# Kernel optimization log

Measured on AMD Instinct MI355X. Metric: run time of the kernel, lower is better.

The kernel has to match this reference:

```python
import jax, jax.numpy as jnp
import numpy as np

T, B = 256, 64
VOCAB, EMBED, HIDDEN, LAYERS, TAGS = 50000, 512, 512, 2, 9
H = HIDDEN // 2  # per-direction hidden size


def setup_inputs() -> dict:
    key = jax.random.key(0)
    ks = jax.random.split(key, 11)
    s = 0.05
    embed_table = jax.random.normal(ks[1], (VOCAB, EMBED), dtype=jnp.float32) * s
    embed_table = embed_table.at[0].set(0.0)  # padding_idx=0 row is zero
    return {
        "x": jax.random.randint(ks[0], (T, B), 1, VOCAB),  # ids >=1 -> full lengths
        "embed_table": embed_table,
        "w_ih": jax.random.normal(ks[2], (LAYERS, 2, 4 * H, HIDDEN), dtype=jnp.float32) * s,
        "w_hh": jax.random.normal(ks[3], (LAYERS, 2, 4 * H, H), dtype=jnp.float32) * s,
        "b_ih": jax.random.normal(ks[4], (LAYERS, 2, 4 * H), dtype=jnp.float32) * s,
        "b_hh": jax.random.normal(ks[5], (LAYERS, 2, 4 * H), dtype=jnp.float32) * s,
        "out_w": jax.random.normal(ks[6], (TAGS, HIDDEN), dtype=jnp.float32) * s,
        "out_b": jax.random.normal(ks[7], (TAGS,), dtype=jnp.float32) * s,
        "start_trans": jax.random.normal(ks[8], (TAGS,), dtype=jnp.float32) * s,
        "end_trans": jax.random.normal(ks[9], (TAGS,), dtype=jnp.float32) * s,
        "trans": jax.random.normal(ks[10], (TAGS, TAGS), dtype=jnp.float32) * s,
    }


def _lstm_dir(xs, Wih, Whh, b, reverse):
    """One LSTM direction over time-major xs [T,B,D]; PyTorch gate order i,f,g,o."""
    bsz = xs.shape[1]
    h0 = jnp.zeros((bsz, H), xs.dtype)
    c0 = jnp.zeros((bsz, H), xs.dtype)

    def step(carry, xt):
        h, c = carry
        g = xt @ Wih.T + h @ Whh.T + b
        i, f, gg, o = jnp.split(g, 4, axis=-1)
        c = jax.nn.sigmoid(f) * c + jax.nn.sigmoid(i) * jnp.tanh(gg)
        h = jax.nn.sigmoid(o) * jnp.tanh(c)
        return (h, c), h

    _, hs = jax.lax.scan(step, (h0, c0), xs, reverse=reverse)
    return hs  # [T,B,H], aligned to input time order


def _emissions(x, embed_table, w_ih, w_hh, b_ih, b_hh, out_w, out_b):
    seq = embed_table[x]  # [T,B,EMBED]
    for l in range(LAYERS):
        fwd = _lstm_dir(seq, w_ih[l, 0], w_hh[l, 0], b_ih[l, 0] + b_hh[l, 0], False)
        bwd = _lstm_dir(seq, w_ih[l, 1], w_hh[l, 1], b_ih[l, 1] + b_hh[l, 1], True)
        seq = jnp.concatenate([fwd, bwd], axis=-1)  # [T,B,HIDDEN]
    return seq @ out_w.T + out_b  # [T,B,TAGS]


def reference(x, embed_table, w_ih, w_hh, b_ih, b_hh, out_w, out_b,
              start_trans, end_trans, trans):
    em = _emissions(x, embed_table, w_ih, w_hh, b_ih, b_hh, out_w, out_b)

    # Viterbi decode (all sequences full-length since ids >= 1)
    score0 = start_trans[None, :] + em[0]  # [B,TAGS]

    def vstep(score, em_t):
        tot = score[:, :, None] + trans[None, :, :]  # [B,prev,cur]
        best_prev = jnp.argmax(tot, axis=1)          # [B,cur]
        return jnp.max(tot, axis=1) + em_t, best_prev

    score, history = jax.lax.scan(vstep, score0, em[1:])  # history: [T-1,B,TAGS]
    score = score + end_trans[None, :]
    best_last = jnp.argmax(score, axis=-1)   # [B]
    best_score = jnp.max(score, axis=-1)     # [B]

    def btstep(tag, idx_t):
        prev = jnp.take_along_axis(idx_t, tag[:, None], axis=1)[:, 0]
        return prev, prev

    _, prevs = jax.lax.scan(btstep, best_last, history, reverse=True)  # [T-1,B]
    tags = jnp.concatenate([prevs, best_last[None, :]], axis=0)        # [T,B]
    return tags.T, best_score  # ([B,T] best paths, [B] path scores)
```

## Files before the change

### kernel.cpp

```cpp
#include <hip/hip_runtime.h>
#include <math.h>

#define TAGS 9

static __device__ __forceinline__ float sigmoidf_(float x) {
  return 1.0f / (1.0f + expf(-x));
}

__device__ __forceinline__ float4 ld4_sc(const float* p) {
  float4 r;
  asm volatile("global_load_dwordx4 %0, %1, off sc0 sc1" : "=v"(r) : "v"(p) : "memory");
  return r;
}
__device__ __forceinline__ void st1_sc(float* p, float v) {
  asm volatile("global_store_dword %0, %1, off sc0 sc1" :: "v"(p), "v"(v) : "memory");
}
__device__ __forceinline__ void waitcnt0() {
  asm volatile("s_waitcnt vmcnt(0)" ::: "memory");
}

__global__ void k_gather(const int* __restrict__ x, const float* __restrict__ table,
                         float* __restrict__ seq) {
  int tid = blockIdx.x * 256 + threadIdx.x;
  int row = tid >> 7;
  int e4 = tid & 127;
  int idx = x[row];
  const float4* src = (const float4*)(table + (size_t)idx * 512);
  float4* dst = (float4*)(seq + (size_t)row * 512);
  dst[e4] = src[e4];
}

__global__ __launch_bounds__(256, 2)
void k_gemm_gates(const float* __restrict__ A, const float* __restrict__ B,
                  const float* __restrict__ bias1, const float* __restrict__ bias2,
                  float* __restrict__ gatesT) {
  __shared__ float As[16][132];
  __shared__ float Bs[16][132];
  int tid = threadIdx.x;
  int tx = tid & 15, ty = tid >> 4;
  int n0 = blockIdx.x * 128, m0 = blockIdx.y * 128;
  int lr = tid >> 2;
  int lk = (tid & 3) * 4;
  float acc[8][8];
#pragma unroll
  for (int i = 0; i < 8; i++)
#pragma unroll
    for (int j = 0; j < 8; j++) acc[i][j] = 0.f;
  const float* Ab = A + (size_t)m0 * 512;
  const float* Bb = B + (size_t)n0 * 512;
  for (int k0 = 0; k0 < 512; k0 += 16) {
    float4 a0 = *(const float4*)&Ab[(size_t)lr * 512 + k0 + lk];
    float4 a1 = *(const float4*)&Ab[(size_t)(lr + 64) * 512 + k0 + lk];
    float4 w0 = *(const float4*)&Bb[(size_t)lr * 512 + k0 + lk];
    float4 w1 = *(const float4*)&Bb[(size_t)(lr + 64) * 512 + k0 + lk];
    __syncthreads();
    As[lk + 0][lr] = a0.x; As[lk + 1][lr] = a0.y; As[lk + 2][lr] = a0.z; As[lk + 3][lr] = a0.w;
    As[lk + 0][lr + 64] = a1.x; As[lk + 1][lr + 64] = a1.y; As[lk + 2][lr + 64] = a1.z; As[lk + 3][lr + 64] = a1.w;
    Bs[lk + 0][lr] = w0.x; Bs[lk + 1][lr] = w0.y; Bs[lk + 2][lr] = w0.z; Bs[lk + 3][lr] = w0.w;
    Bs[lk + 0][lr + 64] = w1.x; Bs[lk + 1][lr + 64] = w1.y; Bs[lk + 2][lr + 64] = w1.z; Bs[lk + 3][lr + 64] = w1.w;
    __syncthreads();
#pragma unroll
    for (int kk = 0; kk < 16; kk++) {
      float4 av0 = *(const float4*)&As[kk][ty * 4];
      float4 av1 = *(const float4*)&As[kk][ty * 4 + 64];
      float4 bv0 = *(const float4*)&Bs[kk][tx * 4];
      float4 bv1 = *(const float4*)&Bs[kk][tx * 4 + 64];
      float am[8] = {av0.x, av0.y, av0.z, av0.w, av1.x, av1.y, av1.z, av1.w};
      float bn[8] = {bv0.x, bv0.y, bv0.z, bv0.w, bv1.x, bv1.y, bv1.z, bv1.w};
#pragma unroll
      for (int i = 0; i < 8; i++)
#pragma unroll
        for (int j = 0; j < 8; j++) acc[i][j] += am[i] * bn[j];
    }
  }
  int t0 = n0 >> 6;
#pragma unroll
  for (int i = 0; i < 8; i++) {
    int m = m0 + ((i < 4) ? (ty * 4 + i) : (64 + ty * 4 + (i - 4)));
    float bs = bias1[m] + bias2[m];
    float4 o0 = {acc[i][0] + bs, acc[i][1] + bs, acc[i][2] + bs, acc[i][3] + bs};
    float4 o1 = {acc[i][4] + bs, acc[i][5] + bs, acc[i][6] + bs, acc[i][7] + bs};
    *(float4*)&gatesT[((size_t)t0 * 2048 + m) * 64 + tx * 4] = o0;
    *(float4*)&gatesT[((size_t)(t0 + 1) * 2048 + m) * 64 + tx * 4] = o1;
  }
}

__global__ __launch_bounds__(512, 1)
void k_lstm_rec(const float* __restrict__ gatesT,
                const float* __restrict__ whh,
                float* __restrict__ seq_out,
                float* __restrict__ hbuf,
                int* __restrict__ arr) {
  __shared__ float h_s[64 * 257];
  __shared__ float w_s[16][256];
  __shared__ float p_s[8][16][64];
  int wg = blockIdx.x, tid = threadIdx.x;
  int d = wg >> 6;
  int u0 = (wg & 63) * 4;
  int b = tid & 63, kq = tid >> 6;
  for (int i = tid; i < 4096; i += 512) {
    int r = i >> 8, k = i & 255;
    int g = r >> 2, uo = r & 3;
    w_s[r][k] = whh[((size_t)d * 1024 + g * 256 + u0 + uo) * 256 + k];
  }
  __syncthreads();
  int uo = tid >> 6;
  float c = 0.f;

  for (int tt = 0; tt < 256; ++tt) {
    int t = d ? 255 - tt : tt;
    float gin0 = 0.f, gin1 = 0.f, gin2 = 0.f, gin3 = 0.f;
    if (tid < 256) {
      const float* gp = gatesT + ((size_t)t * 2048 + d * 1024 + u0 + uo) * 64 + b;
      gin0 = gp[0 * 16384];
      gin1 = gp[1 * 16384];
      gin2 = gp[2 * 16384];
      gin3 = gp[3 * 16384];
    }
    const float* hcur = hbuf + (size_t)(tt & 1) * 32768 + (size_t)d * 16384;
    float4 hv[8];
#pragma unroll
    for (int i = 0; i < 8; i++) hv[i] = ld4_sc(hcur + (size_t)(tid + i * 512) * 4);
    waitcnt0();
#pragma unroll
    for (int i = 0; i < 8; i++) {
      int f = tid + i * 512;
      float* hp = &h_s[(f >> 6) * 257 + (f & 63) * 4];
      hp[0] = hv[i].x; hp[1] = hv[i].y; hp[2] = hv[i].z; hp[3] = hv[i].w;
    }
    __syncthreads();
    float pr[16];
#pragma unroll
    for (int r = 0; r < 16; r++) pr[r] = 0.f;
    const int hb = b * 257 + kq * 32;
#pragma unroll
    for (int j = 0; j < 8; j++) {
      float h0 = h_s[hb + j * 4 + 0], h1 = h_s[hb + j * 4 + 1];
      float h2 = h_s[hb + j * 4 + 2], h3 = h_s[hb + j * 4 + 3];
#pragma unroll
      for (int r = 0; r < 16; r++) {
        float4 w = *(const float4*)&w_s[r][kq * 32 + j * 4];
        pr[r] += w.x * h0 + w.y * h1 + w.z * h2 + w.w * h3;
      }
    }
#pragma unroll
    for (int r = 0; r < 16; r++) p_s[kq][r][b] = pr[r];
    __syncthreads();
    if (tid < 256) {
      float gv[4] = {gin0, gin1, gin2, gin3};
#pragma unroll
      for (int g = 0; g < 4; g++) {
        int r = g * 4 + uo;
        float s = gv[g];
#pragma unroll
        for (int q = 0; q < 8; q++) s += p_s[q][r][b];
        gv[g] = s;
      }
      c = sigmoidf_(gv[1]) * c + sigmoidf_(gv[0]) * tanhf(gv[2]);
      float h = sigmoidf_(gv[3]) * tanhf(c);
      float* hnext = hbuf + (size_t)((tt + 1) & 1) * 32768 + (size_t)d * 16384;
      st1_sc(hnext + b * 256 + u0 + uo, h);
      seq_out[((size_t)t * 64 + b) * 512 + d * 256 + u0 + uo] = h;
    }
    if (tt < 255) {
      waitcnt0();
      __syncthreads();
      if (tid == 0) {
        int* ap = arr + ((size_t)d * 256 + tt) * 4;
        __hip_atomic_fetch_add(&ap[wg & 3], 1, __ATOMIC_RELAXED, __HIP_MEMORY_SCOPE_AGENT);
        while (true) {
          int s = __hip_atomic_load(&ap[0], __ATOMIC_RELAXED, __HIP_MEMORY_SCOPE_AGENT)
                + __hip_atomic_load(&ap[1], __ATOMIC_RELAXED, __HIP_MEMORY_SCOPE_AGENT)
                + __hip_atomic_load(&ap[2], __ATOMIC_RELAXED, __HIP_MEMORY_SCOPE_AGENT)
                + __hip_atomic_load(&ap[3], __ATOMIC_RELAXED, __HIP_MEMORY_SCOPE_AGENT);
          if (s >= 64) break;
          __builtin_amdgcn_s_sleep(1);
        }
      }
      __syncthreads();
    }
  }
}

__global__ void k_emis(const float* __restrict__ seq, const float* __restrict__ out_w,
                       const float* __restrict__ out_b, float* __restrict__ em) {
  __shared__ float ow[TAGS * 512];
  int tid = threadIdx.x;
  for (int i = tid; i < TAGS * 512; i += 256) ow[i] = out_w[i];
  __syncthreads();
  int lane = tid & 63;
  int row = blockIdx.x * 4 + (tid >> 6);
  const float* s = seq + (size_t)row * 512;
  float p[TAGS];
#pragma unroll
  for (int t = 0; t < TAGS; t++) p[t] = 0.f;
#pragma unroll
  for (int kk = 0; kk < 8; kk++) {
    float sv = s[lane + kk * 64];
#pragma unroll
    for (int t = 0; t < TAGS; t++) p[t] += sv * ow[t * 512 + lane + kk * 64];
  }
#pragma unroll
  for (int t = 0; t < TAGS; t++) {
    float v = p[t];
#pragma unroll
    for (int off = 32; off > 0; off >>= 1) v += __shfl_down(v, off, 64);
    if (lane == 0) em[(size_t)row * TAGS + t] = v + out_b[t];
  }
}

__global__ void k_viterbi(const float* __restrict__ em, const float* __restrict__ start_t,
                          const float* __restrict__ end_t, const float* __restrict__ trans,
                          float* __restrict__ out) {
  int b = blockIdx.x;
  int lane = threadIdx.x;
  __shared__ unsigned char hist[255 * TAGS];
  float tin[TAGS];
#pragma unroll
  for (int p = 0; p < TAGS; p++) tin[p] = (lane < TAGS) ? trans[p * TAGS + lane] : 0.f;
  float score = -1e30f;
  if (lane < TAGS) score = start_t[lane] + em[(size_t)b * TAGS + lane];
  for (int t = 1; t < 256; t++) {
    float best = -1e30f; int bp = 0;
#pragma unroll
    for (int p = 0; p < TAGS; p++) {
      float v = __shfl(score, p, 64) + tin[p];
      if (v > best) { best = v; bp = p; }
    }
    if (lane < TAGS) {
      score = best + em[(size_t)(t * 64 + b) * TAGS + lane];
      hist[(t - 1) * TAGS + lane] = (unsigned char)bp;
    }
  }
  float fin = (lane < TAGS) ? (score + end_t[lane]) : -1e30f;
  float bsc = -1e30f; int bl = 0;
#pragma unroll
  for (int p = 0; p < TAGS; p++) {
    float v = __shfl(fin, p, 64);
    if (v > bsc) { bsc = v; bl = p; }
  }
  __syncthreads();
  if (lane == 0) {
    out[(size_t)16384 + b] = bsc;
    int tag = bl;
    out[(size_t)b * 256 + 255] = (float)tag;
    for (int t = 254; t >= 0; t--) {
      tag = hist[t * TAGS + tag];
      out[(size_t)b * 256 + t] = (float)tag;
    }
  }
}

extern "C" void kernel_launch(void* const* d_in, const int* in_sizes, int n_in,
                              void* d_out, int out_size, void* d_ws, size_t ws_size,
                              hipStream_t stream) {
  const int*   x       = (const int*)d_in[0];
  const float* table   = (const float*)d_in[1];
  const float* w_ih    = (const float*)d_in[2];
  const float* w_hh    = (const float*)d_in[3];
  const float* b_ih    = (const float*)d_in[4];
  const float* b_hh    = (const float*)d_in[5];
  const float* out_w   = (const float*)d_in[6];
  const float* out_b   = (const float*)d_in[7];
  const float* start_t = (const float*)d_in[8];
  const float* end_t   = (const float*)d_in[9];
  const float* trans   = (const float*)d_in[10];
  float* out = (float*)d_out;
  float* ws = (float*)d_ws;

  float* seq0   = ws;
  float* seq1   = seq0 + 8388608;
  float* gatesT = seq1 + 8388608;
  float* em     = gatesT + 33554432;
  float* hbufA  = em + 147456;
  float* hbufB  = hbufA + 65536;
  int*   arrA   = (int*)(hbufB + 65536);
  int*   arrB   = arrA + 2048;

  hipMemsetAsync(arrA, 0, 4096 * sizeof(int), stream);
  hipMemsetAsync(hbufA, 0, 32768 * sizeof(float), stream);
  hipMemsetAsync(hbufB, 0, 32768 * sizeof(float), stream);

  k_gather<<<8192, 256, 0, stream>>>(x, table, seq0);

  dim3 gg(128, 16);
  k_gemm_gates<<<gg, 256, 0, stream>>>(w_ih, seq0, b_ih, b_hh, gatesT);
  k_lstm_rec<<<128, 512, 0, stream>>>(gatesT, w_hh, seq1, hbufA, arrA);
  k_gemm_gates<<<gg, 256, 0, stream>>>(w_ih + 1048576, seq1, b_ih + 2048, b_hh + 2048, gatesT);
  k_lstm_rec<<<128, 512, 0, stream>>>(gatesT, w_hh + 524288, seq0, hbufB, arrB);
  k_emis<<<4096, 256, 0, stream>>>(seq0, out_w, out_b, em);
  k_viterbi<<<64, 64, 0, stream>>>(em, start_t, end_t, trans, out);
}
```

Baseline: 5.366 ms.

## Use channel-major sequence layout, register-resident h, and prepacked recurrent weights

Switches the inter-layer sequence buffers to a channel-major (transposed) layout, so the gate GEMM loads B tiles with coalesced float4 rows and the emission kernel reads one column per thread. In the recurrent kernel, each thread now loads its own h slice straight into registers from a transposed h buffer, and reads prepacked W_hh from global/L1 instead of staging both through LDS. This removes one barrier and the LDS transpose per timestep, and the cross-block barrier shrinks to a single counter. The trade-off is an added W_hh pack kernel, an uncoalesced transposed write in the gather, and a per-step weight read from cache rather than LDS.

```diff
diff --git a/kernel.cpp b/kernel.cpp
--- a/kernel.cpp
+++ b/kernel.cpp
@@ -7,9 +7,9 @@
   return 1.0f / (1.0f + expf(-x));
 }
 
-__device__ __forceinline__ float4 ld4_sc(const float* p) {
-  float4 r;
-  asm volatile("global_load_dwordx4 %0, %1, off sc0 sc1" : "=v"(r) : "v"(p) : "memory");
+__device__ __forceinline__ float ld1_sc(const float* p) {
+  float r;
+  asm volatile("global_load_dword %0, %1, off sc0 sc1" : "=v"(r) : "v"(p) : "memory");
   return r;
 }
 __device__ __forceinline__ void st1_sc(float* p, float v) {
@@ -19,19 +19,52 @@
   asm volatile("s_waitcnt vmcnt(0)" ::: "memory");
 }
 
-__global__ void k_gather(const int* __restrict__ x, const float* __restrict__ table,
-                         float* __restrict__ seq) {
-  int tid = blockIdx.x * 256 + threadIdx.x;
-  int row = tid >> 7;
-  int e4 = tid & 127;
-  int idx = x[row];
-  const float4* src = (const float4*)(table + (size_t)idx * 512);
-  float4* dst = (float4*)(seq + (size_t)row * 512);
-  dst[e4] = src[e4];
+__global__ void k_pack_w(const float* __restrict__ whh, float* __restrict__ wPack) {
+  int i = blockIdx.x * 256 + threadIdx.x;
+  int rr = i & 15;
+  int k = (i >> 4) & 255;
+  int wg = (i >> 12) & 127;
+  int L = i >> 19;
+  int d = wg >> 6, ug = wg & 63;
+  int row = d * 1024 + (rr >> 2) * 256 + ug * 4 + (rr & 3);
+  wPack[i] = whh[(size_t)L * 524288 + (size_t)row * 256 + k];
+}
+
+__global__ void k_pack_ow(const float* __restrict__ out_w, float* __restrict__ owT) {
+  int i = blockIdx.x * 256 + threadIdx.x;
+  int tag = i % 9, ch = i / 9;
+  owT[ch * 12 + tag] = out_w[tag * 512 + ch];
+}
+
+__global__ __launch_bounds__(256, 1)
+void k_gatherT(const int* __restrict__ x, const float* __restrict__ table,
+               float* __restrict__ seqT) {
+  __shared__ float tile[64 * 513];
+  __shared__ int x_s[64];
+  int wg = blockIdx.x;
+  int tid = threadIdx.x;
+  int tb0 = wg * 64;
+  if (tid < 64) x_s[tid] = x[tb0 + tid];
+  __syncthreads();
+#pragma unroll
+  for (int i = 0; i < 32; i++) {
+    int idx = tid + i * 256;
+    int r = idx >> 7, c4 = (idx & 127) * 4;
+    float4 v = *(const float4*)&table[(size_t)x_s[r] * 512 + c4];
+    float* tp = &tile[r * 513 + c4];
+    tp[0] = v.x; tp[1] = v.y; tp[2] = v.z; tp[3] = v.w;
+  }
+  __syncthreads();
+#pragma unroll
+  for (int i = 0; i < 128; i++) {
+    int j = tid + i * 256;
+    int ch = j >> 6, b = j & 63;
+    seqT[(size_t)ch * 16384 + tb0 + b] = tile[b * 513 + ch];
+  }
 }
 
 __global__ __launch_bounds__(256, 2)
-void k_gemm_gates(const float* __restrict__ A, const float* __restrict__ B,
+void k_gemm_gates(const float* __restrict__ A, const float* __restrict__ seqT,
                   const float* __restrict__ bias1, const float* __restrict__ bias2,
                   float* __restrict__ gatesT) {
   __shared__ float As[16][132];
@@ -41,23 +74,24 @@
   int n0 = blockIdx.x * 128, m0 = blockIdx.y * 128;
   int lr = tid >> 2;
   int lk = (tid & 3) * 4;
+  int bkk = tid >> 4, bn8 = (tid & 15) * 8;
   float acc[8][8];
 #pragma unroll
   for (int i = 0; i < 8; i++)
 #pragma unroll
     for (int j = 0; j < 8; j++) acc[i][j] = 0.f;
   const float* Ab = A + (size_t)m0 * 512;
-  const float* Bb = B + (size_t)n0 * 512;
   for (int k0 = 0; k0 < 512; k0 += 16) {
     float4 a0 = *(const float4*)&Ab[(size_t)lr * 512 + k0 + lk];
     float4 a1 = *(const float4*)&Ab[(size_t)(lr + 64) * 512 + k0 + lk];
-    float4 w0 = *(const float4*)&Bb[(size_t)lr * 512 + k0 + lk];
-    float4 w1 = *(const float4*)&Bb[(size_t)(lr + 64) * 512 + k0 + lk];
+    const float* Bp = seqT + (size_t)(k0 + bkk) * 16384 + n0 + bn8;
+    float4 b0 = *(const float4*)Bp;
+    float4 b1 = *(const float4*)(Bp + 4);
     __syncthreads();
     As[lk + 0][lr] = a0.x; As[lk + 1][lr] = a0.y; As[lk + 2][lr] = a0.z; As[lk + 3][lr] = a0.w;
     As[lk + 0][lr + 64] = a1.x; As[lk + 1][lr + 64] = a1.y; As[lk + 2][lr + 64] = a1.z; As[lk + 3][lr + 64] = a1.w;
-    Bs[lk + 0][lr] = w0.x; Bs[lk + 1][lr] = w0.y; Bs[lk + 2][lr] = w0.z; Bs[lk + 3][lr] = w0.w;
-    Bs[lk + 0][lr + 64] = w1.x; Bs[lk + 1][lr + 64] = w1.y; Bs[lk + 2][lr + 64] = w1.z; Bs[lk + 3][lr + 64] = w1.w;
+    *(float4*)&Bs[bkk][bn8] = b0;
+    *(float4*)&Bs[bkk][bn8 + 4] = b1;
     __syncthreads();
 #pragma unroll
     for (int kk = 0; kk < 16; kk++) {
@@ -87,24 +121,19 @@
 
 __global__ __launch_bounds__(512, 1)
 void k_lstm_rec(const float* __restrict__ gatesT,
-                const float* __restrict__ whh,
-                float* __restrict__ seq_out,
+                const float* __restrict__ wPack,
+                const float* __restrict__ whh_unused,
+                float* __restrict__ seqT_out,
                 float* __restrict__ hbuf,
                 int* __restrict__ arr) {
-  __shared__ float h_s[64 * 257];
-  __shared__ float w_s[16][256];
-  __shared__ float p_s[8][16][64];
+  __shared__ float p_s[8 * 16 * 64];
   int wg = blockIdx.x, tid = threadIdx.x;
   int d = wg >> 6;
   int u0 = (wg & 63) * 4;
-  int b = tid & 63, kq = tid >> 6;
-  for (int i = tid; i < 4096; i += 512) {
-    int r = i >> 8, k = i & 255;
-    int g = r >> 2, uo = r & 3;
-    w_s[r][k] = whh[((size_t)d * 1024 + g * 256 + u0 + uo) * 256 + k];
-  }
-  __syncthreads();
+  int b = tid & 63;
+  int kq = __builtin_amdgcn_readfirstlane(tid >> 6);
   int uo = tid >> 6;
+  const float4* wp4 = (const float4*)(wPack + ((size_t)wg * 256 + kq * 32) * 16);
   float c = 0.f;
 
   for (int tt = 0; tt < 256; ++tt) {
@@ -117,96 +146,77 @@
       gin2 = gp[2 * 16384];
       gin3 = gp[3 * 16384];
     }
-    const float* hcur = hbuf + (size_t)(tt & 1) * 32768 + (size_t)d * 16384;
-    float4 hv[8];
-#pragma unroll
-    for (int i = 0; i < 8; i++) hv[i] = ld4_sc(hcur + (size_t)(tid + i * 512) * 4);
+    const float* hcur = hbuf + (size_t)(tt & 1) * 32768 + (size_t)d * 16384 + kq * 32 * 64 + b;
+    float hreg[32];
+#pragma unroll
+    for (int j = 0; j < 32; j++) hreg[j] = ld1_sc(hcur + j * 64);
     waitcnt0();
-#pragma unroll
-    for (int i = 0; i < 8; i++) {
-      int f = tid + i * 512;
-      float* hp = &h_s[(f >> 6) * 257 + (f & 63) * 4];
-      hp[0] = hv[i].x; hp[1] = hv[i].y; hp[2] = hv[i].z; hp[3] = hv[i].w;
-    }
-    __syncthreads();
-    float pr[16];
-#pragma unroll
-    for (int r = 0; r < 16; r++) pr[r] = 0.f;
-    const int hb = b * 257 + kq * 32;
-#pragma unroll
-    for (int j = 0; j < 8; j++) {
-      float h0 = h_s[hb + j * 4 + 0], h1 = h_s[hb + j * 4 + 1];
-      float h2 = h_s[hb + j * 4 + 2], h3 = h_s[hb + j * 4 + 3];
-#pragma unroll
-      for (int r = 0; r < 16; r++) {
-        float4 w = *(const float4*)&w_s[r][kq * 32 + j * 4];
-        pr[r] += w.x * h0 + w.y * h1 + w.z * h2 + w.w * h3;
-      }
-    }
-#pragma unroll
-    for (int r = 0; r < 16; r++) p_s[kq][r][b] = pr[r];
+    float acc[16];
+#pragma unroll
+    for (int r = 0; r < 16; r++) acc[r] = 0.f;
+#pragma unroll 8
+    for (int j = 0; j < 32; j++) {
+      float hj = hreg[j];
+      float4 w0 = wp4[j * 4 + 0];
+      float4 w1 = wp4[j * 4 + 1];
+      float4 w2 = wp4[j * 4 + 2];
+      float4 w3 = wp4[j * 4 + 3];
+      acc[0] += w0.x * hj;  acc[1] += w0.y * hj;  acc[2] += w0.z * hj;  acc[3] += w0.w * hj;
+      acc[4] += w1.x * hj;  acc[5] += w1.y * hj;  acc[6] += w1.z * hj;  acc[7] += w1.w * hj;
+      acc[8] += w2.x * hj;  acc[9] += w2.y * hj;  acc[10] += w2.z * hj; acc[11] += w2.w * hj;
+      acc[12] += w3.x * hj; acc[13] += w3.y * hj; acc[14] += w3.z * hj; acc[15] += w3.w * hj;
+    }
+#pragma unroll
+    for (int r = 0; r < 16; r++) p_s[(kq * 16 + r) * 64 + b] = acc[r];
     __syncthreads();
     if (tid < 256) {
       float gv[4] = {gin0, gin1, gin2, gin3};
 #pragma unroll
       for (int g = 0; g < 4; g++) {
-        int r = g * 4 + uo;
+        int rr = g * 4 + uo;
         float s = gv[g];
 #pragma unroll
-        for (int q = 0; q < 8; q++) s += p_s[q][r][b];
+        for (int q = 0; q < 8; q++) s += p_s[(q * 16 + rr) * 64 + b];
         gv[g] = s;
       }
       c = sigmoidf_(gv[1]) * c + sigmoidf_(gv[0]) * tanhf(gv[2]);
       float h = sigmoidf_(gv[3]) * tanhf(c);
       float* hnext = hbuf + (size_t)((tt + 1) & 1) * 32768 + (size_t)d * 16384;
-      st1_sc(hnext + b * 256 + u0 + uo, h);
-      seq_out[((size_t)t * 64 + b) * 512 + d * 256 + u0 + uo] = h;
+      st1_sc(hnext + (u0 + uo) * 64 + b, h);
+      seqT_out[(size_t)(d * 256 + u0 + uo) * 16384 + t * 64 + b] = h;
     }
     if (tt < 255) {
       waitcnt0();
       __syncthreads();
       if (tid == 0) {
-        int* ap = arr + ((size_t)d * 256 + tt) * 4;
-        __hip_atomic_fetch_add(&ap[wg & 3], 1, __ATOMIC_RELAXED, __HIP_MEMORY_SCOPE_AGENT);
-        while (true) {
-          int s = __hip_atomic_load(&ap[0], __ATOMIC_RELAXED, __HIP_MEMORY_SCOPE_AGENT)
-                + __hip_atomic_load(&ap[1], __ATOMIC_RELAXED, __HIP_MEMORY_SCOPE_AGENT)
-                + __hip_atomic_load(&ap[2], __ATOMIC_RELAXED, __HIP_MEMORY_SCOPE_AGENT)
-                + __hip_atomic_load(&ap[3], __ATOMIC_RELAXED, __HIP_MEMORY_SCOPE_AGENT);
-          if (s >= 64) break;
-          __builtin_amdgcn_s_sleep(1);
-        }
+        int* ap = arr + d * 256 + tt;
+        __hip_atomic_fetch_add(ap, 1, __ATOMIC_RELAXED, __HIP_MEMORY_SCOPE_AGENT);
+        while (__hip_atomic_load(ap, __ATOMIC_RELAXED, __HIP_MEMORY_SCOPE_AGENT) < 64)
+          __builtin_amdgcn_s_sleep(2);
       }
       __syncthreads();
     }
   }
 }
 
-__global__ void k_emis(const float* __restrict__ seq, const float* __restrict__ out_w,
-                       const float* __restrict__ out_b, float* __restrict__ em) {
-  __shared__ float ow[TAGS * 512];
-  int tid = threadIdx.x;
-  for (int i = tid; i < TAGS * 512; i += 256) ow[i] = out_w[i];
-  __syncthreads();
-  int lane = tid & 63;
-  int row = blockIdx.x * 4 + (tid >> 6);
-  const float* s = seq + (size_t)row * 512;
+__global__ __launch_bounds__(256, 4)
+void k_emis(const float* __restrict__ seqT, const float* __restrict__ owT,
+            const float* __restrict__ out_b, float* __restrict__ em) {
+  int tb = blockIdx.x * 256 + threadIdx.x;
   float p[TAGS];
 #pragma unroll
   for (int t = 0; t < TAGS; t++) p[t] = 0.f;
-#pragma unroll
-  for (int kk = 0; kk < 8; kk++) {
-    float sv = s[lane + kk * 64];
-#pragma unroll
-    for (int t = 0; t < TAGS; t++) p[t] += sv * ow[t * 512 + lane + kk * 64];
-  }
-#pragma unroll
-  for (int t = 0; t < TAGS; t++) {
-    float v = p[t];
-#pragma unroll
-    for (int off = 32; off > 0; off >>= 1) v += __shfl_down(v, off, 64);
-    if (lane == 0) em[(size_t)row * TAGS + t] = v + out_b[t];
-  }
+  for (int ch = 0; ch < 512; ch++) {
+    float sv = seqT[(size_t)ch * 16384 + tb];
+    const float4* o4 = (const float4*)(owT + ch * 12);
+    float4 oa = o4[0], ob = o4[1];
+    float oc = owT[ch * 12 + 8];
+    p[0] += sv * oa.x; p[1] += sv * oa.y; p[2] += sv * oa.z; p[3] += sv * oa.w;
+    p[4] += sv * ob.x; p[5] += sv * ob.y; p[6] += sv * ob.z; p[7] += sv * ob.w;
+    p[8] += sv * oc;
+  }
+#pragma unroll
+  for (int t = 0; t < TAGS; t++) em[(size_t)tb * TAGS + t] = p[t] + out_b[t];
 }
 
 __global__ void k_viterbi(const float* __restrict__ em, const float* __restrict__ start_t,
@@ -268,26 +278,29 @@
   float* out = (float*)d_out;
   float* ws = (float*)d_ws;
 
-  float* seq0   = ws;
-  float* seq1   = seq0 + 8388608;
-  float* gatesT = seq1 + 8388608;
-  float* em     = gatesT + 33554432;
-  float* hbufA  = em + 147456;
+  float* seqT0  = ws;
+  float* seqT1  = seqT0 + 8388608;
+  float* gatesT = seqT1 + 8388608;
+  float* em     = gatesT;
+  float* hbufA  = gatesT + 33554432;
   float* hbufB  = hbufA + 65536;
-  int*   arrA   = (int*)(hbufB + 65536);
-  int*   arrB   = arrA + 2048;
-
-  hipMemsetAsync(arrA, 0, 4096 * sizeof(int), stream);
+  float* wPack  = hbufB + 65536;
+  float* owT    = wPack + 1048576;
+  int*   arr    = (int*)(owT + 6144);
+
+  hipMemsetAsync(arr, 0, 1024 * sizeof(int), stream);
   hipMemsetAsync(hbufA, 0, 32768 * sizeof(float), stream);
   hipMemsetAsync(hbufB, 0, 32768 * sizeof(float), stream);
 
-  k_gather<<<8192, 256, 0, stream>>>(x, table, seq0);
+  k_pack_w<<<4096, 256, 0, stream>>>(w_hh, wPack);
+  k_pack_ow<<<18, 256, 0, stream>>>(out_w, owT);
+  k_gatherT<<<256, 256, 0, stream>>>(x, table, seqT0);
 
   dim3 gg(128, 16);
-  k_gemm_gates<<<gg, 256, 0, stream>>>(w_ih, seq0, b_ih, b_hh, gatesT);
-  k_lstm_rec<<<128, 512, 0, stream>>>(gatesT, w_hh, seq1, hbufA, arrA);
-  k_gemm_gates<<<gg, 256, 0, stream>>>(w_ih + 1048576, seq1, b_ih + 2048, b_hh + 2048, gatesT);
-  k_lstm_rec<<<128, 512, 0, stream>>>(gatesT, w_hh + 524288, seq0, hbufB, arrB);
-  k_emis<<<4096, 256, 0, stream>>>(seq0, out_w, out_b, em);
+  k_gemm_gates<<<gg, 256, 0, stream>>>(w_ih, seqT0, b_ih, b_hh, gatesT);
+  k_lstm_rec<<<128, 512, 0, stream>>>(gatesT, wPack, w_hh, seqT1, hbufA, arr);
+  k_gemm_gates<<<gg, 256, 0, stream>>>(w_ih + 1048576, seqT1, b_ih + 2048, b_hh + 2048, gatesT);
+  k_lstm_rec<<<128, 512, 0, stream>>>(gatesT, wPack + 524288, w_hh, seqT0, hbufB, arr + 512);
+  k_emis<<<64, 256, 0, stream>>>(seqT0, owT, out_b, em);
   k_viterbi<<<64, 64, 0, stream>>>(em, start_t, end_t, trans, out);
 }
```

Result: faster. 4.961 ms (-7.5%).
